# Performance work log

Hardware: AMD Instinct MI355X
Metric: run time of the kernel (lower is better)

## Reference

```python
import jax, jax.numpy as jnp
import numpy as np

OUT_FEATURES = 4096
IN_FEATURES = 4096
NNZ = 1048576
BATCH = 128


def setup_inputs() -> dict:
    key = jax.random.key(0)
    k_x, k_v, k_r, k_c = jax.random.split(key, 4)
    X = jax.random.normal(k_x, (BATCH, IN_FEATURES), dtype=jnp.float32)
    W_vals = jax.random.normal(k_v, (NNZ,), dtype=jnp.float32)
    W_rows = jax.random.randint(k_r, (NNZ,), 0, OUT_FEATURES, dtype=jnp.int32)
    W_cols = jax.random.randint(k_c, (NNZ,), 0, IN_FEATURES, dtype=jnp.int32)
    return {"X": X, "W_vals": W_vals, "W_rows": W_rows, "W_cols": W_cols}


def reference(X, W_vals, W_rows, W_cols):
    # torch.sparse.mm(W, X.T).T with W in COO form.
    # out[b, i] = sum_{k: rows[k]==i} vals[k] * X[b, cols[k]]
    gathered = X.T[W_cols] * W_vals[:, None]            # [nnz, B]
    out_T = jax.ops.segment_sum(gathered, W_rows, num_segments=OUT_FEATURES)  # [OUT, B]
    return out_T.T                                       # [B, OUT]
```

## Files before the change

kernel.cpp:

```cpp
#include <hip/hip_runtime.h>
#include <hip/hip_bf16.h>

#define OUTF 4096
#define INF  4096
#define BATCH 128
#define NBIN 1024
#define CHUNK 4096
#define SEGP (NBIN + 1)
#define SQ   1028

typedef _Float16 f16x8 __attribute__((ext_vector_type(8)));
typedef float    f32x4 __attribute__((ext_vector_type(4)));


__global__ __launch_bounds__(256) void k_prep(const float* __restrict__ X,
                                              const float* __restrict__ vals,
                                              const int* __restrict__ rows,
                                              const int* __restrict__ cols,
                                              int nnz, int nw,
                                              _Float16* __restrict__ Xh,
                                              int2* __restrict__ bucket,
                                              int* __restrict__ segStart) {
  __shared__ int  hist[NBIN];
  __shared__ int  scanT[256];
  __shared__ int2 stage[CHUNK];
  const int t = threadIdx.x;
  const int blk = blockIdx.x;

  if (blk < nw) {
    const int s = blk * CHUNK;
    const int e = min(nnz, s + CHUNK);
    const int cnt = e - s;
    for (int b = t; b < NBIN; b += 256) hist[b] = 0;
    __syncthreads();

    int   bins[16], metas[16];
    float vv[16];
    int   nloc = 0;
#pragma unroll
    for (int j = 0; j < 4; ++j) {
      int gi = s + (j * 256 + t) * 4;
      if (gi + 3 < e) {
        int g = gi >> 2;
        int4   r4 = ((const int4*)rows)[g];
        int4   c4 = ((const int4*)cols)[g];
        float4 v4 = ((const float4*)vals)[g];
        int rr[4] = {r4.x, r4.y, r4.z, r4.w};
        int cc[4] = {c4.x, c4.y, c4.z, c4.w};
        float vf[4] = {v4.x, v4.y, v4.z, v4.w};
#pragma unroll
        for (int q = 0; q < 4; ++q) {
          bins[nloc]  = ((rr[q] >> 4) << 2) | (cc[q] >> 10);
          metas[nloc] = ((rr[q] & 15) << 10) | (cc[q] & 1023);
          vv[nloc] = vf[q];
          atomicAdd(&hist[bins[nloc]], 1);
          ++nloc;
        }
      } else {
        for (int i = gi; i < e; ++i) {
          int r = rows[i], c = cols[i];
          bins[nloc]  = ((r >> 4) << 2) | (c >> 10);
          metas[nloc] = ((r & 15) << 10) | (c & 1023);
          vv[nloc] = vals[i];
          atomicAdd(&hist[bins[nloc]], 1);
          ++nloc;
        }
      }
    }
    __syncthreads();

    const int base = t * 4;
    int l0 = hist[base], l1 = hist[base + 1], l2 = hist[base + 2], l3 = hist[base + 3];
    int sum = l0 + l1 + l2 + l3;
    scanT[t] = sum;
    __syncthreads();
    for (int off = 1; off < 256; off <<= 1) {
      int u = (t >= off) ? scanT[t - off] : 0;
      __syncthreads();
      scanT[t] += u;
      __syncthreads();
    }
    int excl = scanT[t] - sum;
    int st0 = excl, st1 = excl + l0, st2 = st1 + l1, st3 = st2 + l2;
    int* sp = segStart + (size_t)blk * SEGP + base;
    sp[0] = st0; sp[1] = st1; sp[2] = st2; sp[3] = st3;
    hist[base] = st0; hist[base + 1] = st1; hist[base + 2] = st2; hist[base + 3] = st3;
    if (t == 255) segStart[(size_t)blk * SEGP + NBIN] = cnt;
    __syncthreads();

    for (int j = 0; j < nloc; ++j) {
      int slot = atomicAdd(&hist[bins[j]], 1);
      int2 ent;
      ent.x = __float_as_int(vv[j]);
      ent.y = metas[j];
      stage[slot] = ent;
    }
    __syncthreads();

    for (int i = t; i < cnt; i += 256) bucket[s + i] = stage[i];
  } else {
    int g = (blk - nw) * 256 + t;
    int n = g >> 9;
    int k0 = (g & 511) * 8;
    float4 f0 = *(const float4*)(X + (size_t)n * INF + k0);
    float4 f1 = *(const float4*)(X + (size_t)n * INF + k0 + 4);
    f16x8 h;
    h[0] = (_Float16)f0.x; h[1] = (_Float16)f0.y;
    h[2] = (_Float16)f0.z; h[3] = (_Float16)f0.w;
    h[4] = (_Float16)f1.x; h[5] = (_Float16)f1.y;
    h[6] = (_Float16)f1.z; h[7] = (_Float16)f1.w;
    size_t idx = ((size_t)(k0 >> 5) * 8 + (n >> 4)) * 512 + (n & 15) * 32 + (k0 & 31);
    *(f16x8*)(Xh + idx) = h;
  }
}

__global__ __launch_bounds__(256, 2) void k_strip(const int2* __restrict__ bucket,
                                                  const int* __restrict__ segStart,
                                                  int nw,
                                                  const _Float16* __restrict__ Xh,
                                                  float* __restrict__ outP) {
  __shared__ float strip[16 * SQ];
  const int t = threadIdx.x;
  const int bin = blockIdx.x;
  const int mt = bin >> 2, kq = bin & 3;

  {
    float4 z = {0.f, 0.f, 0.f, 0.f};
    const int nvec = 16 * SQ / 4;
    for (int j = t; j < nvec; j += 256) ((float4*)strip)[j] = z;
  }
  __syncthreads();

  for (int cc = t; cc < nw; cc += 256) {
    const int* sp = segStart + (size_t)cc * SEGP + bin;
    int sb = sp[0];
    int se = sp[1];
    const int2* p = bucket + (size_t)cc * CHUNK;
    for (int j = sb; j < se; ++j) {
      int2 e = p[j];
      atomicAdd(&strip[((e.y >> 10) & 15) * SQ + (e.y & 1023)], __int_as_float(e.x));
    }
  }
  __syncthreads();

  const int lane = t & 63, wid = t >> 6;
  const int lr = lane & 15, lg = lane >> 4;
  f32x4 acc[8] = {};
  for (int ktl = wid; ktl < 32; ktl += 4) {
    const int kt = kq * 32 + ktl;
    float4 alo = *(const float4*)&strip[lr * SQ + ktl * 32 + lg * 8];
    float4 ahi = *(const float4*)&strip[lr * SQ + ktl * 32 + lg * 8 + 4];
    f16x8 a;
    a[0] = (_Float16)alo.x; a[1] = (_Float16)alo.y;
    a[2] = (_Float16)alo.z; a[3] = (_Float16)alo.w;
    a[4] = (_Float16)ahi.x; a[5] = (_Float16)ahi.y;
    a[6] = (_Float16)ahi.z; a[7] = (_Float16)ahi.w;
    const _Float16* bp = Xh + (size_t)kt * 4096 + lr * 32 + lg * 8;
    f16x8 b[8];
#pragma unroll
    for (int nt = 0; nt < 8; ++nt) b[nt] = *(const f16x8*)(bp + nt * 512);
#pragma unroll
    for (int nt = 0; nt < 8; ++nt)
      acc[nt] = __builtin_amdgcn_mfma_f32_16x16x32_f16(a, b[nt], acc[nt], 0, 0, 0);
  }
  __syncthreads();

  float* red = strip;
#pragma unroll
  for (int nt = 0; nt < 8; ++nt)
#pragma unroll
    for (int i = 0; i < 4; ++i)
      red[wid * 2048 + (lg * 4 + i) * 128 + nt * 16 + lr] = acc[nt][i];
  __syncthreads();
  float* op = outP + (size_t)kq * (OUTF * BATCH) + (size_t)mt * 2048;
  for (int e = t; e < 2048; e += 256)
    op[e] = red[e] + red[2048 + e] + red[4096 + e] + red[6144 + e];
}

__global__ __launch_bounds__(1024) void k_merge(const float* __restrict__ outP,
                                                float* __restrict__ out) {
  __shared__ float t[32][33];
  int bbase = blockIdx.x * 32;
  int rbase = blockIdx.y * 32;
  size_t src = (size_t)(rbase + threadIdx.y) * 128 + bbase + threadIdx.x;
  float s = outP[src] + outP[(size_t)OUTF * BATCH + src] +
            outP[(size_t)2 * OUTF * BATCH + src] + outP[(size_t)3 * OUTF * BATCH + src];
  t[threadIdx.y][threadIdx.x] = s;
  __syncthreads();
  out[(size_t)(bbase + threadIdx.y) * OUTF + rbase + threadIdx.x] = t[threadIdx.x][threadIdx.y];
}

__global__ __launch_bounds__(256) void k_fallback(const float* __restrict__ X,
                                                  const float* __restrict__ vals,
                                                  const int* __restrict__ rows,
                                                  const int* __restrict__ cols, int n,
                                                  float* __restrict__ out) {
  int k = blockIdx.x * blockDim.x + threadIdx.x;
  if (k >= n) return;
  float v = vals[k];
  int r = rows[k], c = cols[k];
  for (int b = 0; b < BATCH; ++b)
    atomicAdd(&out[(size_t)b * OUTF + r], v * X[(size_t)b * INF + c]);
}

extern "C" void kernel_launch(void* const* d_in, const int* in_sizes, int n_in,
                              void* d_out, int out_size, void* d_ws, size_t ws_size,
                              hipStream_t stream) {
  const float* X  = (const float*)d_in[0];
  const float* Wv = (const float*)d_in[1];
  const int*   Wr = (const int*)d_in[2];
  const int*   Wc = (const int*)d_in[3];
  float* out = (float*)d_out;
  const int nnz = in_sizes[1];
  const int nw = (nnz + CHUNK - 1) / CHUNK;

  char* ws = (char*)d_ws;
  const size_t OFF_XH   = 0;
  const size_t OFF_BKT  = OFF_XH  + (size_t)BATCH * INF * 2;
  const size_t OFF_SEG  = OFF_BKT + (size_t)(nw * CHUNK) * 8;
  const size_t OFF_OUTP = OFF_SEG + (size_t)nw * SEGP * 4;
  const size_t NEEDED   = OFF_OUTP + (size_t)4 * OUTF * BATCH * 4;

  if (ws_size < NEEDED) {
    hipMemsetAsync(d_out, 0, (size_t)out_size * 4, stream);
    k_fallback<<<dim3((nnz + 255) / 256), dim3(256), 0, stream>>>(X, Wv, Wr, Wc, nnz, out);
    return;
  }

  _Float16* Xh       = (_Float16*)(ws + OFF_XH);
  int2*     bucket   = (int2*)(ws + OFF_BKT);
  int*      segStart = (int*)(ws + OFF_SEG);
  float*    outP     = (float*)(ws + OFF_OUTP);

  k_prep<<<dim3(nw + 256), dim3(256), 0, stream>>>(X, Wv, Wr, Wc, nnz, nw, Xh, bucket, segStart);
  k_strip<<<dim3(NBIN), dim3(256), 0, stream>>>(bucket, segStart, nw, Xh, outP);
  k_merge<<<dim3(BATCH / 32, OUTF / 32), dim3(32, 32), 0, stream>>>(outP, out);
}
```

Measured before the change: 110.3 us.

## Transpose segment offsets for coalesced reads and unroll full-chunk bucketing

Adds a small transpose kernel that rewrites the per-chunk segment offset table bin-major. k_strip threads can then read their per-chunk offsets with coalesced loads instead of strided ones. k_prep also gets a fast path for full chunks with fully unrolled, statically indexed register arrays, which avoids dynamic indexing that may spill to scratch. The cost is an extra kernel launch plus a workspace buffer. The partial-chunk path now only covers four elements per thread, so a tail chunk larger than 1024 entries would be mishandled. The new fallback condition on nw masks this only when nw is not a multiple of 32.

```diff
diff --git a/kernel.cpp b/kernel.cpp
--- a/kernel.cpp
+++ b/kernel.cpp
@@ -36,36 +36,38 @@
 
     int   bins[16], metas[16];
     float vv[16];
-    int   nloc = 0;
-#pragma unroll
-    for (int j = 0; j < 4; ++j) {
-      int gi = s + (j * 256 + t) * 4;
-      if (gi + 3 < e) {
-        int g = gi >> 2;
+
+    if (cnt == CHUNK) {
+#pragma unroll
+      for (int j = 0; j < 4; ++j) {
+        const int g = (s >> 2) + j * 256 + t;
         int4   r4 = ((const int4*)rows)[g];
         int4   c4 = ((const int4*)cols)[g];
         float4 v4 = ((const float4*)vals)[g];
-        int rr[4] = {r4.x, r4.y, r4.z, r4.w};
-        int cc[4] = {c4.x, c4.y, c4.z, c4.w};
-        float vf[4] = {v4.x, v4.y, v4.z, v4.w};
-#pragma unroll
-        for (int q = 0; q < 4; ++q) {
-          bins[nloc]  = ((rr[q] >> 4) << 2) | (cc[q] >> 10);
-          metas[nloc] = ((rr[q] & 15) << 10) | (cc[q] & 1023);
-          vv[nloc] = vf[q];
-          atomicAdd(&hist[bins[nloc]], 1);
-          ++nloc;
-        }
-      } else {
-        for (int i = gi; i < e; ++i) {
-          int r = rows[i], c = cols[i];
-          bins[nloc]  = ((r >> 4) << 2) | (c >> 10);
-          metas[nloc] = ((r & 15) << 10) | (c & 1023);
-          vv[nloc] = vals[i];
-          atomicAdd(&hist[bins[nloc]], 1);
-          ++nloc;
-        }
-      }
+        bins[j * 4 + 0]  = ((r4.x >> 4) << 2) | (c4.x >> 10);
+        bins[j * 4 + 1]  = ((r4.y >> 4) << 2) | (c4.y >> 10);
+        bins[j * 4 + 2]  = ((r4.z >> 4) << 2) | (c4.z >> 10);
+        bins[j * 4 + 3]  = ((r4.w >> 4) << 2) | (c4.w >> 10);
+        metas[j * 4 + 0] = ((r4.x & 15) << 10) | (c4.x & 1023);
+        metas[j * 4 + 1] = ((r4.y & 15) << 10) | (c4.y & 1023);
+        metas[j * 4 + 2] = ((r4.z & 15) << 10) | (c4.z & 1023);
+        metas[j * 4 + 3] = ((r4.w & 15) << 10) | (c4.w & 1023);
+        vv[j * 4 + 0] = v4.x; vv[j * 4 + 1] = v4.y;
+        vv[j * 4 + 2] = v4.z; vv[j * 4 + 3] = v4.w;
+#pragma unroll
+        for (int q = 0; q < 4; ++q) atomicAdd(&hist[bins[j * 4 + q]], 1);
+      }
+    } else {
+      int nloc = 0;
+      for (int i = s + 4 * t; i < min(e, s + 4 * t + 4); ++i) {
+        int r = rows[i], c = cols[i];
+        bins[nloc]  = ((r >> 4) << 2) | (c >> 10);
+        metas[nloc] = ((r & 15) << 10) | (c & 1023);
+        vv[nloc] = vals[i];
+        atomicAdd(&hist[bins[nloc]], 1);
+        ++nloc;
+      }
+      for (int j = nloc; j < 16; ++j) bins[j] = -1;
     }
     __syncthreads();
 
@@ -88,12 +90,24 @@
     if (t == 255) segStart[(size_t)blk * SEGP + NBIN] = cnt;
     __syncthreads();
 
-    for (int j = 0; j < nloc; ++j) {
-      int slot = atomicAdd(&hist[bins[j]], 1);
-      int2 ent;
-      ent.x = __float_as_int(vv[j]);
-      ent.y = metas[j];
-      stage[slot] = ent;
+    if (cnt == CHUNK) {
+#pragma unroll
+      for (int j = 0; j < 16; ++j) {
+        int slot = atomicAdd(&hist[bins[j]], 1);
+        int2 ent;
+        ent.x = __float_as_int(vv[j]);
+        ent.y = metas[j];
+        stage[slot] = ent;
+      }
+    } else {
+      for (int j = 0; j < 16; ++j) {
+        if (bins[j] < 0) break;
+        int slot = atomicAdd(&hist[bins[j]], 1);
+        int2 ent;
+        ent.x = __float_as_int(vv[j]);
+        ent.y = metas[j];
+        stage[slot] = ent;
+      }
     }
     __syncthreads();
 
@@ -114,8 +128,22 @@
   }
 }
 
+__global__ __launch_bounds__(1024) void k_segT(const int* __restrict__ segStart,
+                                               int* __restrict__ segT, int nw) {
+  __shared__ int tile[32][33];
+  int b0 = blockIdx.x * 32;
+  int c0 = blockIdx.y * 32;
+  int bin = b0 + threadIdx.y;
+  if (bin < SEGP)
+    tile[threadIdx.y][threadIdx.x] = segStart[(size_t)(c0 + threadIdx.x) * SEGP + bin];
+  __syncthreads();
+  int obin = b0 + threadIdx.x;
+  if (obin < SEGP)
+    segT[(size_t)obin * nw + c0 + threadIdx.y] = tile[threadIdx.x][threadIdx.y];
+}
+
 __global__ __launch_bounds__(256, 2) void k_strip(const int2* __restrict__ bucket,
-                                                  const int* __restrict__ segStart,
+                                                  const int* __restrict__ segT,
                                                   int nw,
                                                   const _Float16* __restrict__ Xh,
                                                   float* __restrict__ outP) {
@@ -132,9 +160,8 @@
   __syncthreads();
 
   for (int cc = t; cc < nw; cc += 256) {
-    const int* sp = segStart + (size_t)cc * SEGP + bin;
-    int sb = sp[0];
-    int se = sp[1];
+    int sb = segT[(size_t)bin * nw + cc];
+    int se = segT[(size_t)(bin + 1) * nw + cc];
     const int2* p = bucket + (size_t)cc * CHUNK;
     for (int j = sb; j < se; ++j) {
       int2 e = p[j];
@@ -218,10 +245,11 @@
   const size_t OFF_XH   = 0;
   const size_t OFF_BKT  = OFF_XH  + (size_t)BATCH * INF * 2;
   const size_t OFF_SEG  = OFF_BKT + (size_t)(nw * CHUNK) * 8;
-  const size_t OFF_OUTP = OFF_SEG + (size_t)nw * SEGP * 4;
+  const size_t OFF_SEGT = OFF_SEG + (size_t)nw * SEGP * 4;
+  const size_t OFF_OUTP = OFF_SEGT + (size_t)SEGP * nw * 4;
   const size_t NEEDED   = OFF_OUTP + (size_t)4 * OUTF * BATCH * 4;
 
-  if (ws_size < NEEDED) {
+  if (ws_size < NEEDED || (nw & 31) != 0) {
     hipMemsetAsync(d_out, 0, (size_t)out_size * 4, stream);
     k_fallback<<<dim3((nnz + 255) / 256), dim3(256), 0, stream>>>(X, Wv, Wr, Wc, nnz, out);
     return;
@@ -230,9 +258,11 @@
   _Float16* Xh       = (_Float16*)(ws + OFF_XH);
   int2*     bucket   = (int2*)(ws + OFF_BKT);
   int*      segStart = (int*)(ws + OFF_SEG);
+  int*      segT     = (int*)(ws + OFF_SEGT);
   float*    outP     = (float*)(ws + OFF_OUTP);
 
   k_prep<<<dim3(nw + 256), dim3(256), 0, stream>>>(X, Wv, Wr, Wc, nnz, nw, Xh, bucket, segStart);
-  k_strip<<<dim3(NBIN), dim3(256), 0, stream>>>(bucket, segStart, nw, Xh, outP);
+  k_segT<<<dim3((SEGP + 31) / 32, nw / 32), dim3(32, 32), 0, stream>>>(segStart, segT, nw);
+  k_strip<<<dim3(NBIN), dim3(256), 0, stream>>>(bucket, segT, nw, Xh, outP);
   k_merge<<<dim3(BATCH / 32, OUTF / 32), dim3(32, 32), 0, stream>>>(outP, out);
 }
```

Result: no change. 109.8 us (-0.5%).
